# Kernel optimization log

Hardware: AMD Instinct MI355X
Metric: run time of the kernel (lower is better)

The kernel has to match this reference:

```python
import jax, jax.numpy as jnp
import numpy as np

NS, NV = 16, 8                 # scalar / vector multiplicities (16x0e + 8x1o)
N_NODES, N_EDGES = 20000, 320000
N_EDGE_FEAT = 64
W_NUMEL = NS*NS + NS*NV + NV*NV + NV*NS   # 576 per-edge TP weights
EPS = 1e-5


def setup_inputs() -> dict:
    key = jax.random.key(0)
    ks = jax.random.split(key, 8)
    D = NS + 3 * NV   # 40
    return {
        "node_attr": jax.random.normal(ks[0], (N_NODES, D), jnp.float32),
        "edge_attr": jax.random.normal(ks[1], (N_EDGES, N_EDGE_FEAT), jnp.float32),
        "edge_sh": jax.random.normal(ks[2], (N_EDGES, 4), jnp.float32),
        "fc1_w": jax.random.normal(ks[3], (N_EDGE_FEAT, N_EDGE_FEAT), jnp.float32) / np.sqrt(N_EDGE_FEAT),
        "fc1_b": jnp.zeros((N_EDGE_FEAT,), jnp.float32),
        "fc2_w": jax.random.normal(ks[4], (N_EDGE_FEAT, W_NUMEL), jnp.float32) / np.sqrt(N_EDGE_FEAT),
        "fc2_b": jnp.zeros((W_NUMEL,), jnp.float32),
        "bn_gamma_s": jnp.ones((NS,), jnp.float32),
        "bn_beta_s": jnp.zeros((NS,), jnp.float32),
        "bn_gamma_v": jnp.ones((NV,), jnp.float32),
        "edge_index": jax.random.randint(ks[5], (2, N_EDGES), 0, N_NODES),
    }


def _tp_conv(node_attr, edge_attr, edge_sh, fc1_w, fc1_b, fc2_w, fc2_b,
             bn_gamma_s, bn_beta_s, bn_gamma_v, edge_index):
    src, dst = edge_index[0], edge_index[1]
    E = edge_attr.shape[0]
    # edge MLP -> flat per-edge tensor-product weights (shared_weights=False)
    h = jax.nn.relu(edge_attr @ fc1_w + fc1_b)
    w = h @ fc2_w + fc2_b                                   # [E, W_NUMEL]
    s0 = NS * NS; s1 = s0 + NS * NV; s2 = s1 + NV * NV
    w1 = w[:, :s0].reshape(E, NS, NS)    # path 0e x 0e -> 0e
    w2 = w[:, s0:s1].reshape(E, NS, NV)  # path 0e x 1o -> 1o
    w3 = w[:, s1:s2].reshape(E, NV, NV)  # path 1o x 0e -> 1o
    w4 = w[:, s2:].reshape(E, NV, NS)    # path 1o x 1o -> 0e
    # gather source node features per edge
    x = node_attr[src]                                      # [E, 40]
    xs = x[:, :NS]                                          # [E, NS]
    xv = x[:, NS:].reshape(E, NV, 3)                        # [E, NV, 3]
    shs = edge_sh[:, 0]                                     # [E] scalar sh
    shv = edge_sh[:, 1:4]                                   # [E, 3] vector sh
    # e3nn-style path normalization: fan-in over paths feeding each output irrep
    a0 = 1.0 / np.sqrt(NS + NV)
    a1 = 1.0 / np.sqrt(NS + NV)
    # CG contraction for 1o x 1o -> 0e (3j symbol = delta / sqrt(3))
    dot = jnp.einsum('eum,em->eu', xv, shv) / np.sqrt(3.0)  # [E, NV]
    out0 = (jnp.einsum('euw,eu->ew', w1, xs) * shs[:, None]
            + jnp.einsum('euw,eu->ew', w4, dot)) * a0       # [E, NS]
    out1 = (jnp.einsum('euw,eu->ew', w2, xs)[:, :, None] * shv[:, None, :]
            + jnp.einsum('euw,eum->ewm', w3, xv) * shs[:, None, None]) * a1  # [E, NV, 3]
    tp = jnp.concatenate([out0, out1.reshape(E, NV * 3)], axis=1)  # [E, 40]
    # scatter-sum to destination nodes (reduce='sum', dim_size=N)
    agg = jax.ops.segment_sum(tp, dst, num_segments=node_attr.shape[0])
    # residual: in/out widths equal -> F.pad is a no-op
    out = agg + node_attr
    # equivariant batch norm: mean/var BN on scalars, norm-only BN on vectors
    os = out[:, :NS]
    ov = out[:, NS:].reshape(-1, NV, 3)
    mu = os.mean(0)
    var = ((os - mu) ** 2).mean(0)
    os = (os - mu) / jnp.sqrt(var + EPS) * bn_gamma_s + bn_beta_s
    vnorm = (ov ** 2).mean(axis=2).mean(axis=0)             # [NV]
    ov = ov / jnp.sqrt(vnorm + EPS)[None, :, None] * bn_gamma_v[None, :, None]
    return jnp.concatenate([os, ov.reshape(-1, NV * 3)], axis=1)


def reference(node_attr, edge_attr, edge_sh, fc1_w, fc1_b, fc2_w, fc2_b,
              bn_gamma_s, bn_beta_s, bn_gamma_v, edge_index):
    return _tp_conv(node_attr, edge_attr, edge_sh, fc1_w, fc1_b, fc2_w, fc2_b,
                    bn_gamma_s, bn_beta_s, bn_gamma_v, edge_index)
```

## Files before the change

### kernel.cpp

```cpp
#include <hip/hip_runtime.h>
#include <stdint.h>


#define E_EDGES   320000
#define N_NODES_C 20000
#define D_C       40
#define A0_C      0.20412414523193154f
#define RSQRT3_C  0.57735026918962576f

typedef __attribute__((ext_vector_type(8))) short        bf16x8;
typedef __attribute__((ext_vector_type(4))) float        f32x4;
typedef __attribute__((ext_vector_type(4))) unsigned int u32x4;
typedef __attribute__((ext_vector_type(4))) int          i32x4;

__device__ __forceinline__ uint32_t rne16(uint32_t u) {
  return (u + 0x7fffu + ((u >> 16) & 1u)) >> 16;
}
__device__ __forceinline__ float4 ld4(const float* p) {
  return *reinterpret_cast<const float4*>(p);
}
__device__ __forceinline__ void st4(float* p, float a, float b, float c, float d) {
  *reinterpret_cast<float4*>(p) = make_float4(a, b, c, d);
}

__device__ __forceinline__ int cjp_map(int jp) {
  return jp < 16 ? jp : (jp < 24 ? jp + 12 : jp - 8);
}

__global__ __launch_bounds__(256) void pack_kernel(
    const float* __restrict__ w2, const float* __restrict__ w1f,
    uint32_t* __restrict__ bpk)
{
  const int tid = blockIdx.x * 256 + threadIdx.x;
  const int frag = tid >> 8;
  const int d    = tid & 255;
  const int lane = d >> 2, q = d & 3;
  const float* W; int stride, col, s;
  if (frag < 216) {
    const int jp = frag / 6; s = frag % 6;
    col = cjp_map(jp) * 16 + (lane & 15); W = w2; stride = 576;
  } else {
    const int f1 = frag - 216; const int nt = f1 / 6; s = f1 % 6;
    col = nt * 16 + (lane & 15); W = w1f; stride = 64;
  }
  uint32_t out = 0;
#pragma unroll
  for (int h = 0; h < 2; ++h) {
    const int t = q * 2 + h;
    const int kk = (lane >> 4) * 8 + t;
    const int krow = (s & 1) * 32 + kk;
    const float v = W[krow * stride + col];
    const uint32_t u = __float_as_uint(v);
    const uint32_t hb = rne16(u);
    uint32_t b16;
    if (s < 4) b16 = hb & 0xffffu;
    else {
      const float lo = v - __uint_as_float(hb << 16);
      b16 = rne16(__float_as_uint(lo)) & 0xffffu;
    }
    out |= b16 << (16 * h);
  }
  bpk[tid] = out;
}

__global__ __launch_bounds__(256, 2) void fc1_mfma_kernel(
    const float* __restrict__ ea, const uint32_t* __restrict__ bpk,
    const float* __restrict__ b1, uint32_t* __restrict__ h2g)
{
  const int tid = threadIdx.x;
  const int w = tid >> 6, lane = tid & 63;
  const int n = lane & 15, g = lane >> 4;
  const int rowB = blockIdx.x * 256 + w * 64;

  bf16x8 Ahi[4][2], Alo[4][2];
#pragma unroll
  for (int mt = 0; mt < 4; ++mt) {
    const int row = rowB + mt * 16 + n;
    const float4* epv = reinterpret_cast<const float4*>(ea + (size_t)row * 64);
#pragma unroll
    for (int s = 0; s < 2; ++s) {
      const float4 fa = epv[s * 8 + g * 2];
      const float4 fb = epv[s * 8 + g * 2 + 1];
      float f[8] = {fa.x, fa.y, fa.z, fa.w, fb.x, fb.y, fb.z, fb.w};
      uint32_t hw[4], lw[4];
#pragma unroll
      for (int j = 0; j < 4; ++j) {
        const uint32_t u0 = __float_as_uint(f[2 * j]);
        const uint32_t u1 = __float_as_uint(f[2 * j + 1]);
        const uint32_t h0 = rne16(u0), h1 = rne16(u1);
        const float l0 = f[2 * j]     - __uint_as_float(h0 << 16);
        const float l1 = f[2 * j + 1] - __uint_as_float(h1 << 16);
        hw[j] = (h0 & 0xffffu) | (h1 << 16);
        lw[j] = (rne16(__float_as_uint(l0)) & 0xffffu) |
                (rne16(__float_as_uint(l1)) << 16);
      }
      u32x4 hv = {hw[0], hw[1], hw[2], hw[3]};
      u32x4 lv = {lw[0], lw[1], lw[2], lw[3]};
      Ahi[mt][s] = __builtin_bit_cast(bf16x8, hv);
      Alo[mt][s] = __builtin_bit_cast(bf16x8, lv);
    }
  }

  const u32x4* bp4 = reinterpret_cast<const u32x4*>(bpk);
#pragma unroll 1
  for (int nt = 0; nt < 4; ++nt) {
    u32x4 bfr[6];
#pragma unroll
    for (int s = 0; s < 6; ++s) bfr[s] = bp4[(216 + nt * 6 + s) * 64 + lane];
    f32x4 acc[4];
#pragma unroll
    for (int mt = 0; mt < 4; ++mt) acc[mt] = (f32x4)(0.0f);
#pragma unroll
    for (int s = 0; s < 6; ++s) {
      const bf16x8 B = __builtin_bit_cast(bf16x8, bfr[s]);
#pragma unroll
      for (int mt = 0; mt < 4; ++mt) {
        const bf16x8 A = (s < 2) ? Ahi[mt][s] : (s < 4 ? Alo[mt][s - 2] : Ahi[mt][s - 4]);
        acc[mt] = __builtin_amdgcn_mfma_f32_16x16x32_bf16(A, B, acc[mt], 0, 0, 0);
      }
    }
    const float bv = b1[nt * 16 + n];
#pragma unroll
    for (int mt = 0; mt < 4; ++mt) {
#pragma unroll
      for (int r = 0; r < 4; ++r) {
        const float v = fmaxf(acc[mt][r] + bv, 0.0f);
        const uint32_t hb = rne16(__float_as_uint(v));
        const float lo = v - __uint_as_float(hb << 16);
        const uint32_t lb = rne16(__float_as_uint(lo)) & 0xffffu;
        const int row = rowB + mt * 16 + g * 4 + r;
        h2g[(size_t)row * 64 + nt * 16 + n] = (hb & 0xffffu) | (lb << 16);
      }
    }
  }
}

__global__ __launch_bounds__(256, 2) void edge_mfma_kernel(
    const uint32_t* __restrict__ h2g, const uint32_t* __restrict__ bpk,
    const float* __restrict__ b2, const float* __restrict__ na,
    const float* __restrict__ sh, const int* __restrict__ ei,
    float* __restrict__ agg)
{
  __shared__ __align__(16) float xsT[4][16][64];
  __shared__ __align__(16) float dtT[4][8][64];
  __shared__ __align__(16) float xvT[4][8][3][64];
  __shared__ __align__(16) float shsT[4][64];
  __shared__ __align__(16) float shvT[4][3][64];
  __shared__ __align__(16) int   dstT[4][64];
  __shared__ float b2s[576];

  const int tid = threadIdx.x;
  const int w = tid >> 6, lane = tid & 63;
  const int n = lane & 15, g = lane >> 4;
  const int eBlock = blockIdx.x * 256;

  {
    const int e = eBlock + tid;
    const int src = ei[e];
    dstT[w][lane] = ei[E_EDGES + e];
    const float4 shq = ld4(sh + (size_t)e * 4);
    shsT[w][lane] = shq.x;
    shvT[w][0][lane] = shq.y; shvT[w][1][lane] = shq.z; shvT[w][2][lane] = shq.w;
    const float* nas = na + (size_t)src * D_C;
    float x[40];
#pragma unroll
    for (int i = 0; i < 10; ++i) {
      const float4 v = ld4(nas + i * 4);
      x[i * 4] = v.x; x[i * 4 + 1] = v.y; x[i * 4 + 2] = v.z; x[i * 4 + 3] = v.w;
    }
#pragma unroll
    for (int u = 0; u < 16; ++u) xsT[w][u][lane] = x[u];
#pragma unroll
    for (int u = 0; u < 8; ++u) {
      const float a = x[16 + u * 3], b = x[16 + u * 3 + 1], c = x[16 + u * 3 + 2];
      xvT[w][u][0][lane] = a; xvT[w][u][1][lane] = b; xvT[w][u][2][lane] = c;
      dtT[w][u][lane] = (a * shq.y + b * shq.z + c * shq.w) * RSQRT3_C;
    }
    if (tid < 144)
      reinterpret_cast<float4*>(b2s)[tid] = reinterpret_cast<const float4*>(b2)[tid];
  }
  __syncthreads();

  bf16x8 Ahi[4][2], Alo[4][2];
#pragma unroll
  for (int mt = 0; mt < 4; ++mt) {
    const int row = eBlock + w * 64 + mt * 16 + n;
    const u32x4* hp = reinterpret_cast<const u32x4*>(h2g + (size_t)row * 64);
#pragma unroll
    for (int s = 0; s < 2; ++s) {
      const u32x4 qa = hp[s * 8 + g * 2];
      const u32x4 qb = hp[s * 8 + g * 2 + 1];
      u32x4 hv, lv;
      hv[0] = (qa[0] & 0xffffu) | (qa[1] << 16);
      hv[1] = (qa[2] & 0xffffu) | (qa[3] << 16);
      hv[2] = (qb[0] & 0xffffu) | (qb[1] << 16);
      hv[3] = (qb[2] & 0xffffu) | (qb[3] << 16);
      lv[0] = (qa[0] >> 16) | (qa[1] & 0xffff0000u);
      lv[1] = (qa[2] >> 16) | (qa[3] & 0xffff0000u);
      lv[2] = (qb[0] >> 16) | (qb[1] & 0xffff0000u);
      lv[3] = (qb[2] >> 16) | (qb[3] & 0xffff0000u);
      Ahi[mt][s] = __builtin_bit_cast(bf16x8, hv);
      Alo[mt][s] = __builtin_bit_cast(bf16x8, lv);
    }
  }

  f32x4 shsv[4]; i32x4 dstv[4];
#pragma unroll
  for (int mt = 0; mt < 4; ++mt) {
    shsv[mt] = *reinterpret_cast<const f32x4*>(&shsT[w][mt * 16 + g * 4]);
    dstv[mt] = *reinterpret_cast<const i32x4*>(&dstT[w][mt * 16 + g * 4]);
  }

  const u32x4* bp4 = reinterpret_cast<const u32x4*>(bpk);

#define TILE_ACC(jp_)                                                          \
  f32x4 acc[4];                                                                \
  {                                                                            \
    u32x4 bfr[6];                                                              \
    _Pragma("unroll")                                                          \
    for (int s = 0; s < 6; ++s) bfr[s] = bp4[((jp_) * 6 + s) * 64 + lane];     \
    _Pragma("unroll")                                                          \
    for (int mt = 0; mt < 4; ++mt) acc[mt] = (f32x4)(0.0f);                    \
    _Pragma("unroll")                                                          \
    for (int s = 0; s < 6; ++s) {                                              \
      const bf16x8 B = __builtin_bit_cast(bf16x8, bfr[s]);                     \
      _Pragma("unroll")                                                        \
      for (int mt = 0; mt < 4; ++mt) {                                         \
        const bf16x8 A = (s < 2) ? Ahi[mt][s]                                  \
                                 : (s < 4 ? Alo[mt][s - 2] : Ahi[mt][s - 4]);  \
        acc[mt] = __builtin_amdgcn_mfma_f32_16x16x32_bf16(A, B, acc[mt], 0, 0, 0); \
      }                                                                        \
    }                                                                          \
    const float bv = b2s[cjp_map(jp_) * 16 + n];                               \
    _Pragma("unroll")                                                          \
    for (int mt = 0; mt < 4; ++mt) acc[mt] = acc[mt] + bv;                     \
  }

  f32x4 out0[4];
#pragma unroll
  for (int mt = 0; mt < 4; ++mt) out0[mt] = (f32x4)(0.0f);
#pragma unroll 4
  for (int jp = 0; jp < 16; ++jp) {
    TILE_ACC(jp);
#pragma unroll
    for (int mt = 0; mt < 4; ++mt) {
      const f32x4 xsv = *reinterpret_cast<const f32x4*>(&xsT[w][jp][mt * 16 + g * 4]);
      out0[mt] += acc[mt] * shsv[mt] * xsv;
    }
  }
#pragma unroll 4
  for (int jp = 16; jp < 24; ++jp) {
    TILE_ACC(jp);
#pragma unroll
    for (int mt = 0; mt < 4; ++mt) {
      const f32x4 dv = *reinterpret_cast<const f32x4*>(&dtT[w][jp - 16][mt * 16 + g * 4]);
      out0[mt] += acc[mt] * dv;
    }
  }
#pragma unroll
  for (int mt = 0; mt < 4; ++mt)
#pragma unroll
    for (int r = 0; r < 4; ++r)
      atomicAdd(&agg[(size_t)dstv[mt][r] * D_C + n], out0[mt][r] * A0_C);

  f32x4 s2[4];
#pragma unroll
  for (int mt = 0; mt < 4; ++mt) s2[mt] = (f32x4)(0.0f);
#pragma unroll 4
  for (int jp = 24; jp < 32; ++jp) {
    TILE_ACC(jp);
    const int u0 = (jp - 24) * 2 + (n >> 3);
#pragma unroll
    for (int mt = 0; mt < 4; ++mt) {
      const f32x4 xsv = *reinterpret_cast<const f32x4*>(&xsT[w][u0][mt * 16 + g * 4]);
      s2[mt] += acc[mt] * xsv;
    }
  }

  f32x4 s3[3][4];
#pragma unroll
  for (int m = 0; m < 3; ++m)
#pragma unroll
    for (int mt = 0; mt < 4; ++mt) s3[m][mt] = (f32x4)(0.0f);
#pragma unroll 2
  for (int jp = 32; jp < 36; ++jp) {
    TILE_ACC(jp);
    const int u0 = (jp - 32) * 2 + (n >> 3);
#pragma unroll
    for (int mt = 0; mt < 4; ++mt)
#pragma unroll
      for (int m = 0; m < 3; ++m) {
        const f32x4 xvv = *reinterpret_cast<const f32x4*>(&xvT[w][u0][m][mt * 16 + g * 4]);
        s3[m][mt] += acc[mt] * xvv;
      }
  }

#pragma unroll
  for (int mt = 0; mt < 4; ++mt)
#pragma unroll
    for (int m = 0; m < 3; ++m) {
      const f32x4 shvv = *reinterpret_cast<const f32x4*>(&shvT[w][m][mt * 16 + g * 4]);
      const f32x4 o = (s2[mt] * shvv + s3[m][mt] * shsv[mt]) * A0_C;
#pragma unroll
      for (int r = 0; r < 4; ++r) {
        float v = o[r];
        v += __shfl_xor(v, 8, 64);
        if (n < 8)
          atomicAdd(&agg[(size_t)dstv[mt][r] * D_C + 16 + n * 3 + m], v);
      }
    }
#undef TILE_ACC
}

__global__ __launch_bounds__(256) void resid_stats_kernel(
    const float* __restrict__ agg, const float* __restrict__ na,
    float* __restrict__ outp, float* __restrict__ stats)
{
  const int nn = blockIdx.x * 256 + threadIdx.x;
  float v[40];
  if (nn < N_NODES_C) {
    const float* ap = agg + (size_t)nn * D_C;
    const float* np = na + (size_t)nn * D_C;
#pragma unroll
    for (int i = 0; i < 10; ++i) {
      const float4 a = ld4(ap + i * 4);
      const float4 b = ld4(np + i * 4);
      v[i * 4] = a.x + b.x; v[i * 4 + 1] = a.y + b.y;
      v[i * 4 + 2] = a.z + b.z; v[i * 4 + 3] = a.w + b.w;
    }
    float* op = outp + (size_t)nn * D_C;
#pragma unroll
    for (int i = 0; i < 10; ++i)
      st4(op + i * 4, v[i * 4], v[i * 4 + 1], v[i * 4 + 2], v[i * 4 + 3]);
  } else {
#pragma unroll
    for (int i = 0; i < 40; ++i) v[i] = 0.f;
  }
  float red[40];
#pragma unroll
  for (int c = 0; c < 16; ++c) { red[c] = v[c]; red[16 + c] = v[c] * v[c]; }
#pragma unroll
  for (int u = 0; u < 8; ++u) {
    const float a = v[16 + u * 3], b = v[16 + u * 3 + 1], c = v[16 + u * 3 + 2];
    red[32 + u] = a * a + b * b + c * c;
  }
#pragma unroll
  for (int i = 0; i < 40; ++i) {
    float x = red[i];
#pragma unroll
    for (int off = 32; off > 0; off >>= 1) x += __shfl_xor(x, off, 64);
    red[i] = x;
  }
  if ((threadIdx.x & 63) == 0) {
#pragma unroll
    for (int i = 0; i < 40; ++i) atomicAdd(stats + i, red[i]);
  }
}

__global__ __launch_bounds__(256) void bn_apply_kernel(
    float* __restrict__ outp, const float* __restrict__ stats,
    const float* __restrict__ gs, const float* __restrict__ bsv,
    const float* __restrict__ gv)
{
  __shared__ float A[16], B[16], AV[8];
  const int tid = threadIdx.x;
  if (tid < 16) {
    const float s = stats[tid], q = stats[16 + tid];
    const float mu = s * (1.f / 20000.f);
    const float var = q * (1.f / 20000.f) - mu * mu;
    const float a = rsqrtf(var + 1e-5f) * gs[tid];
    A[tid] = a;
    B[tid] = bsv[tid] - mu * a;
  } else if (tid < 24) {
    const int u = tid - 16;
    const float vn = stats[32 + u] * (1.f / (20000.f * 3.f));
    AV[u] = rsqrtf(vn + 1e-5f) * gv[u];
  }
  __syncthreads();
  const int nn = blockIdx.x * 256 + tid;
  if (nn < N_NODES_C) {
    float* op = outp + (size_t)nn * D_C;
    float v[40];
#pragma unroll
    for (int i = 0; i < 10; ++i) {
      const float4 t = ld4(op + i * 4);
      v[i * 4] = t.x; v[i * 4 + 1] = t.y; v[i * 4 + 2] = t.z; v[i * 4 + 3] = t.w;
    }
#pragma unroll
    for (int c = 0; c < 16; ++c) v[c] = v[c] * A[c] + B[c];
#pragma unroll
    for (int u = 0; u < 8; ++u) {
      const float a = AV[u];
      v[16 + u * 3] *= a; v[16 + u * 3 + 1] *= a; v[16 + u * 3 + 2] *= a;
    }
#pragma unroll
    for (int i = 0; i < 10; ++i)
      st4(op + i * 4, v[i * 4], v[i * 4 + 1], v[i * 4 + 2], v[i * 4 + 3]);
  }
}

extern "C" void kernel_launch(void* const* d_in, const int* in_sizes, int n_in,
                              void* d_out, int out_size, void* d_ws, size_t ws_size,
                              hipStream_t stream) {
  const float* node_attr = (const float*)d_in[0];
  const float* edge_attr = (const float*)d_in[1];
  const float* edge_sh   = (const float*)d_in[2];
  const float* fc1_w     = (const float*)d_in[3];
  const float* fc1_b     = (const float*)d_in[4];
  const float* fc2_w     = (const float*)d_in[5];
  const float* fc2_b     = (const float*)d_in[6];
  const float* gs        = (const float*)d_in[7];
  const float* bs        = (const float*)d_in[8];
  const float* gv        = (const float*)d_in[9];
  const int*   ei        = (const int*)d_in[10];
  float* out = (float*)d_out;

  char* ws = (char*)d_ws;
  uint32_t* h2   = (uint32_t*)(ws);
  float*    agg  = (float*)(ws + 81920000);
  float*    stats= (float*)(ws + 81920000 + 3200000);
  uint32_t* bpk  = (uint32_t*)d_out;

  hipMemsetAsync(agg, 0, 3200000 + 160, stream);
  pack_kernel<<<240, 256, 0, stream>>>(fc2_w, fc1_w, bpk);
  fc1_mfma_kernel<<<1250, 256, 0, stream>>>(edge_attr, bpk, fc1_b, h2);
  edge_mfma_kernel<<<1250, 256, 0, stream>>>(h2, bpk, fc2_b, node_attr, edge_sh, ei, agg);
  resid_stats_kernel<<<79, 256, 0, stream>>>(agg, node_attr, out, stats);
  bn_apply_kernel<<<79, 256, 0, stream>>>(out, stats, gs, bs, gv);
}
```

Before: 450.7 us.

## Alias edge-kernel LDS buffers and raise launch bounds to four blocks per CU

The xs, dot and xv shared-memory arrays are folded into one reused buffer. The vector features are reloaded from global memory into the space freed after the scalar passes, which needs two extra block barriers. This cuts the LDS footprint, and both fc1 and the edge kernel now request four resident blocks per CU instead of two. The goal is higher occupancy to hide gather and atomic latency, at the cost of a second node-feature gather, extra syncs, and tighter register limits that could cause spills.

```diff
diff --git a/kernel.cpp b/kernel.cpp
--- a/kernel.cpp
+++ b/kernel.cpp
@@ -63,7 +63,7 @@
   bpk[tid] = out;
 }
 
-__global__ __launch_bounds__(256, 2) void fc1_mfma_kernel(
+__global__ __launch_bounds__(256, 4) void fc1_mfma_kernel(
     const float* __restrict__ ea, const uint32_t* __restrict__ bpk,
     const float* __restrict__ b1, uint32_t* __restrict__ h2g)
 {
@@ -135,15 +135,13 @@
   }
 }
 
-__global__ __launch_bounds__(256, 2) void edge_mfma_kernel(
+__global__ __launch_bounds__(256, 4) void edge_mfma_kernel(
     const uint32_t* __restrict__ h2g, const uint32_t* __restrict__ bpk,
     const float* __restrict__ b2, const float* __restrict__ na,
     const float* __restrict__ sh, const int* __restrict__ ei,
     float* __restrict__ agg)
 {
-  __shared__ __align__(16) float xsT[4][16][64];
-  __shared__ __align__(16) float dtT[4][8][64];
-  __shared__ __align__(16) float xvT[4][8][3][64];
+  __shared__ __align__(16) float ubuf[6144];
   __shared__ __align__(16) float shsT[4][64];
   __shared__ __align__(16) float shvT[4][3][64];
   __shared__ __align__(16) int   dstT[4][64];
@@ -154,9 +152,9 @@
   const int n = lane & 15, g = lane >> 4;
   const int eBlock = blockIdx.x * 256;
 
+  const int e = eBlock + tid;
+  const int src = ei[e];
   {
-    const int e = eBlock + tid;
-    const int src = ei[e];
     dstT[w][lane] = ei[E_EDGES + e];
     const float4 shq = ld4(sh + (size_t)e * 4);
     shsT[w][lane] = shq.x;
@@ -169,12 +167,12 @@
       x[i * 4] = v.x; x[i * 4 + 1] = v.y; x[i * 4 + 2] = v.z; x[i * 4 + 3] = v.w;
     }
 #pragma unroll
-    for (int u = 0; u < 16; ++u) xsT[w][u][lane] = x[u];
+    for (int u = 0; u < 16; ++u) ubuf[(w * 16 + u) * 64 + lane] = x[u];
 #pragma unroll
     for (int u = 0; u < 8; ++u) {
       const float a = x[16 + u * 3], b = x[16 + u * 3 + 1], c = x[16 + u * 3 + 2];
-      xvT[w][u][0][lane] = a; xvT[w][u][1][lane] = b; xvT[w][u][2][lane] = c;
-      dtT[w][u][lane] = (a * shq.y + b * shq.z + c * shq.w) * RSQRT3_C;
+      ubuf[4096 + (w * 8 + u) * 64 + lane] =
+          (a * shq.y + b * shq.z + c * shq.w) * RSQRT3_C;
     }
     if (tid < 144)
       reinterpret_cast<float4*>(b2s)[tid] = reinterpret_cast<const float4*>(b2)[tid];
@@ -244,7 +242,8 @@
     TILE_ACC(jp);
 #pragma unroll
     for (int mt = 0; mt < 4; ++mt) {
-      const f32x4 xsv = *reinterpret_cast<const f32x4*>(&xsT[w][jp][mt * 16 + g * 4]);
+      const f32x4 xsv = *reinterpret_cast<const f32x4*>(
+          &ubuf[(w * 16 + jp) * 64 + mt * 16 + g * 4]);
       out0[mt] += acc[mt] * shsv[mt] * xsv;
     }
   }
@@ -253,7 +252,8 @@
     TILE_ACC(jp);
 #pragma unroll
     for (int mt = 0; mt < 4; ++mt) {
-      const f32x4 dv = *reinterpret_cast<const f32x4*>(&dtT[w][jp - 16][mt * 16 + g * 4]);
+      const f32x4 dv = *reinterpret_cast<const f32x4*>(
+          &ubuf[4096 + (w * 8 + (jp - 16)) * 64 + mt * 16 + g * 4]);
       out0[mt] += acc[mt] * dv;
     }
   }
@@ -272,10 +272,28 @@
     const int u0 = (jp - 24) * 2 + (n >> 3);
 #pragma unroll
     for (int mt = 0; mt < 4; ++mt) {
-      const f32x4 xsv = *reinterpret_cast<const f32x4*>(&xsT[w][u0][mt * 16 + g * 4]);
+      const f32x4 xsv = *reinterpret_cast<const f32x4*>(
+          &ubuf[(w * 16 + u0) * 64 + mt * 16 + g * 4]);
       s2[mt] += acc[mt] * xsv;
     }
   }
+
+  __syncthreads();
+  {
+    const float* nav = na + (size_t)src * D_C + 16;
+    float xv[24];
+#pragma unroll
+    for (int i = 0; i < 6; ++i) {
+      const float4 v = ld4(nav + i * 4);
+      xv[i * 4] = v.x; xv[i * 4 + 1] = v.y; xv[i * 4 + 2] = v.z; xv[i * 4 + 3] = v.w;
+    }
+#pragma unroll
+    for (int u = 0; u < 8; ++u)
+#pragma unroll
+      for (int m = 0; m < 3; ++m)
+        ubuf[((w * 8 + u) * 3 + m) * 64 + lane] = xv[u * 3 + m];
+  }
+  __syncthreads();
 
   f32x4 s3[3][4];
 #pragma unroll
@@ -290,7 +308,8 @@
     for (int mt = 0; mt < 4; ++mt)
 #pragma unroll
       for (int m = 0; m < 3; ++m) {
-        const f32x4 xvv = *reinterpret_cast<const f32x4*>(&xvT[w][u0][m][mt * 16 + g * 4]);
+        const f32x4 xvv = *reinterpret_cast<const f32x4*>(
+            &ubuf[((w * 8 + u0) * 3 + m) * 64 + mt * 16 + g * 4]);
         s3[m][mt] += acc[mt] * xvv;
       }
   }
```

Measured after the change: 613.3 us. +36.1%, slower.
